# Kernel tuning notes

Measured on AMD Instinct MI355X. Metric: run time of the kernel, lower is better.

## Reference

```python
import jax, jax.numpy as jnp
import numpy as np

B, N, C, K, RPE = 8, 4096, 256, 16, 64
LN_EPS = 1e-5


def _layernorm(x, g, b):
    m = jnp.mean(x, axis=-1, keepdims=True)
    v = jnp.mean((x - m) ** 2, axis=-1, keepdims=True)
    return (x - m) * jax.lax.rsqrt(v + LN_EPS) * g + b


def setup_inputs() -> dict:
    key = jax.random.key(0)
    ks = jax.random.split(key, 10)
    def w(k, shape, s=0.02):
        return jax.random.normal(k, shape, jnp.float32) * s
    return {
        "x": jax.random.normal(ks[0], (B, N, C), jnp.float32),
        "pos": jax.random.normal(ks[1], (B, N, 3), jnp.float32),
        "Wq": w(ks[2], (C, C)),
        "Wk": w(ks[3], (C, C)),
        "Wv": w(ks[4], (C, C)),
        "W1": w(ks[5], (3, RPE)), "b1": jnp.zeros((RPE,), jnp.float32),
        "W2": w(ks[6], (RPE, C)), "b2": jnp.zeros((C,), jnp.float32),
        "Wp": w(ks[7], (C, C)), "bp": jnp.zeros((C,), jnp.float32),
        "gq": jnp.ones((C,), jnp.float32), "betaq": jnp.zeros((C,), jnp.float32),
        "gkv": jnp.ones((C,), jnp.float32), "betakv": jnp.zeros((C,), jnp.float32),
    }


def reference(x, pos, Wq, Wk, Wv, W1, b1, W2, b2, Wp, bp, gq, betaq, gkv, betakv):
    scale = C ** (-0.5)
    x_q = _layernorm(x, gq, betaq)
    x_kv = _layernorm(x, gkv, betakv)
    q = x_q @ Wq                      # (B,N,C)
    k = x_kv @ Wk                     # (B,N,C)
    v = x_kv @ Wv                     # (B,N,C)

    # kNN over squared pairwise distances (self has distance 0 on the diagonal)
    a2 = jnp.sum(pos * pos, axis=-1)                       # (B,N)
    dist2 = a2[:, :, None] + a2[:, None, :] - 2.0 * jnp.einsum(
        "bnc,bmc->bnm", pos, pos)                          # (B,N,N)
    dist2 = jnp.maximum(dist2, 0.0)
    eye = jnp.eye(N, dtype=bool)
    dist2 = jnp.where(eye[None], 0.0, dist2)
    _, idx = jax.lax.top_k(-dist2, K)                      # (B,N,K) smallest-k

    gather = jax.vmap(lambda f, i: f[i])                   # (N,C),(N,K)->(N,K,C)
    k_nb = gather(k, idx)                                  # (B,N,K,C)
    v_nb = gather(v, idx)                                  # (B,N,K,C)
    pos_nb = gather(pos, idx)                              # (B,N,K,3)

    rel = pos[:, :, None, :] - pos_nb                      # (B,N,K,3)
    rel_enc = jax.nn.relu(rel @ W1 + b1) @ W2 + b2         # (B,N,K,C)

    attn_logits = jnp.einsum("bnc,bnkc->bnk", q, k_nb) * scale
    attn_logits = attn_logits + jnp.sum(rel_enc, axis=-1) * scale
    attn = jax.nn.softmax(attn_logits, axis=-1)            # (B,N,K)

    out = jnp.einsum("bnk,bnkc->bnc", attn, v_nb)
    out = out @ Wp + bp
    return out
```

## Files before the change

### kernel.cpp

```cpp
#include <hip/hip_runtime.h>
#include <hip/hip_bf16.h>
#include <stdint.h>

#define Bv 8
#define Nv 4096
#define Cv 256
#define Kv 16
#define RPEv 64
#define CAPv 160

typedef short bf16x8 __attribute__((ext_vector_type(8)));
typedef float f32x4 __attribute__((ext_vector_type(4)));
typedef _Float16 half2v __attribute__((ext_vector_type(2)));
typedef unsigned short u16x2 __attribute__((ext_vector_type(2)));

static __device__ __forceinline__ float bf2f(unsigned int u16) {
    union { unsigned int i; float f; } v; v.i = u16 << 16; return v.f;
}
static __device__ __forceinline__ unsigned short f2bf(float f) {
    union { float f; unsigned int i; } v; v.f = f;
    unsigned int x = v.i;
    return (unsigned short)((x + 0x7fffu + ((x >> 16) & 1u)) >> 16);
}
static __device__ __forceinline__ unsigned int umin32(unsigned int a, unsigned int b) { return a < b ? a : b; }
static __device__ __forceinline__ unsigned int umax32(unsigned int a, unsigned int b) { return a > b ? a : b; }
static __device__ __forceinline__ unsigned short f2h(float f) {
    _Float16 h = (_Float16)f; return __builtin_bit_cast(unsigned short, h);
}
static __device__ __forceinline__ float h2f(unsigned int u) {
    _Float16 h = __builtin_bit_cast(_Float16, (unsigned short)(u & 0xffffu)); return (float)h;
}
static __device__ __forceinline__ half2v bch2(unsigned int u) { return __builtin_bit_cast(half2v, u); }
static __device__ __forceinline__ unsigned int bcu32(u16x2 v) { return __builtin_bit_cast(unsigned int, v); }

__global__ __launch_bounds__(256) void pre_kernel(
    const float* __restrict__ x,
    const float* __restrict__ gq, const float* __restrict__ bq,
    const float* __restrict__ gkv, const float* __restrict__ bkv,
    unsigned short* __restrict__ Aq, unsigned short* __restrict__ Akv,
    const float* __restrict__ Wq, const float* __restrict__ Wk,
    const float* __restrict__ Wv, const float* __restrict__ Wp,
    unsigned short* __restrict__ Bt,
    const float* __restrict__ W2, const float* __restrict__ b2,
    float* __restrict__ w2sum, float* __restrict__ b2sum)
{
    const int bid = blockIdx.x;
    const int tid = threadIdx.x;
    if (bid < 4096) {
        const long r0 = (long)bid * 8;
        const int row = tid >> 5;
        const int c0 = (tid & 31) * 8;
        const float* xr = x + (r0 + row) * Cv + c0;
        float xv[8];
        *(float4*)&xv[0] = *(const float4*)xr;
        *(float4*)&xv[4] = *(const float4*)(xr + 4);
        float s = 0.f, s2 = 0.f;
#pragma unroll
        for (int i = 0; i < 8; ++i) { s += xv[i]; s2 = fmaf(xv[i], xv[i], s2); }
#pragma unroll
        for (int m = 16; m >= 1; m >>= 1) { s += __shfl_xor(s, m); s2 += __shfl_xor(s2, m); }
        const float mean = s * (1.f / Cv);
        const float var = fmaf(-mean, mean, s2 * (1.f / Cv));
        const float rs = rsqrtf(fmaxf(var, 0.f) + 1e-5f);
        unsigned int pq[4], pk[4];
#pragma unroll
        for (int i = 0; i < 4; ++i) {
            const int c = c0 + 2 * i;
            const float h0 = (xv[2 * i] - mean) * rs;
            const float h1 = (xv[2 * i + 1] - mean) * rs;
            const unsigned int q0 = f2bf(fmaf(h0, gq[c], bq[c]));
            const unsigned int q1 = f2bf(fmaf(h1, gq[c + 1], bq[c + 1]));
            const unsigned int k0 = f2bf(fmaf(h0, gkv[c], bkv[c]));
            const unsigned int k1 = f2bf(fmaf(h1, gkv[c + 1], bkv[c + 1]));
            pq[i] = q0 | (q1 << 16);
            pk[i] = k0 | (k1 << 16);
        }
        const long off = (r0 + row) * Cv + c0;
        *(uint4*)&Aq[off]  = make_uint4(pq[0], pq[1], pq[2], pq[3]);
        *(uint4*)&Akv[off] = make_uint4(pk[0], pk[1], pk[2], pk[3]);
    } else if (bid < 5120) {
        const int r = bid - 4096;
        const float* W = (r < 256) ? Wq : (r < 512) ? Wk : (r < 768) ? Wv : Wp;
        const int n = r & 255;
        Bt[r * 256 + tid] = f2bf(W[tid * 256 + n]);
    } else {
        if (tid < RPEv) {
            float s = 0.f;
            for (int c = 0; c < Cv; ++c) s += W2[tid * Cv + c];
            w2sum[tid] = s;
        }
        if (tid == 0) {
            float s = 0.f;
            for (int c = 0; c < Cv; ++c) s += b2[c];
            *b2sum = s;
        }
    }
}

__global__ __launch_bounds__(256) void gemmknn_kernel(
    const float* __restrict__ pos, int* __restrict__ idx_out,
    const unsigned short* __restrict__ Aq, const unsigned short* __restrict__ Akv,
    const unsigned short* __restrict__ Bt,
    unsigned short* __restrict__ qo, unsigned short* __restrict__ ko,
    unsigned short* __restrict__ vo)
{
    __shared__ char smem[65536] __attribute__((aligned(16)));
    const int tid = threadIdx.x;
    const int bid = blockIdx.x;

    if (bid < 1024) {
        uint2* pxy2 = (uint2*)smem;
        unsigned int* pz2 = (unsigned int*)(smem + 16384);
        uint4* qu = (uint4*)(smem + 24576);
        unsigned int* akeys = (unsigned int*)(smem + 25088);
        unsigned int* cnt = (unsigned int*)(smem + 28160);
        unsigned short* bufs = (unsigned short*)(smem + 28288);

        const int ql = tid >> 3;
        const int s  = tid & 7;
        const int q  = bid * 32 + ql;
        const int b  = q >> 12;
        const int n  = q & (Nv - 1);
        const float* pb = pos + (size_t)b * Nv * 3;

        for (int i = tid; i < Nv / 2; i += 256) {
            const float* pp = pb + 6 * i;
            const float2 u0 = *(const float2*)pp;
            const float2 u1 = *(const float2*)(pp + 2);
            const float2 u2 = *(const float2*)(pp + 4);
            const unsigned int x0 = f2h(u0.x), y0 = f2h(u0.y), z0 = f2h(u1.x);
            const unsigned int x1 = f2h(u1.y), y1 = f2h(u2.x), z1 = f2h(u2.y);
            pxy2[i] = make_uint2(x0 | (x1 << 16), y0 | (y1 << 16));
            pz2[i] = z0 | (z1 << 16);
        }
        __syncthreads();

        const int pq = n >> 1;
        const int hq = (n & 1) * 16;
        const uint2 qxy = pxy2[pq];
        const unsigned int qzz = pz2[pq];
        const unsigned int hx = (qxy.x >> hq) & 0xffffu;
        const unsigned int hy = (qxy.y >> hq) & 0xffffu;
        const unsigned int hz = (qzz   >> hq) & 0xffffu;
        const half2v qxp = bch2(hx | (hx << 16));
        const half2v qyp = bch2(hy | (hy << 16));
        const half2v qzp = bch2(hz | (hz << 16));

        u16x2 ch0 = {0x7c00, 0x7c00}, ch1 = ch0, ch2 = ch0;
        for (int t = 0; t < 256; ++t) {
            const int p = 8 * t + s;
            const uint2 xy = pxy2[p];
            const unsigned int zz = pz2[p];
            const half2v dx = bch2(xy.x) - qxp;
            const half2v dy = bch2(xy.y) - qyp;
            const half2v dz = bch2(zz) - qzp;
            const half2v d2 = dx * dx + dy * dy + dz * dz;
            const u16x2 k = __builtin_bit_cast(u16x2, d2);
            const u16x2 mn0 = __builtin_elementwise_min(ch0, k);
            const u16x2 mx0 = __builtin_elementwise_max(ch0, k);
            ch0 = mn0;
            const u16x2 mn1 = __builtin_elementwise_min(ch1, mx0);
            const u16x2 mx1 = __builtin_elementwise_max(ch1, mx0);
            ch1 = mn1;
            ch2 = __builtin_elementwise_min(ch2, mx1);
        }
        akeys[tid * 3 + 0] = bcu32(ch0);
        akeys[tid * 3 + 1] = bcu32(ch1);
        akeys[tid * 3 + 2] = bcu32(ch2);
        __syncthreads();

        if (tid < 32) {
            unsigned int sel16[16];
#pragma unroll
            for (int i = 0; i < 16; ++i) sel16[i] = 0xFFFFFFFFu;
            for (int s8 = 0; s8 < 8; ++s8) {
#pragma unroll
                for (int i3 = 0; i3 < 3; ++i3) {
                    const unsigned int v = akeys[(8 * tid + s8) * 3 + i3];
#pragma unroll
                    for (int h = 0; h < 2; ++h) {
                        unsigned int cand = (h == 0) ? (v & 0xffffu) : (v >> 16);
                        if (cand < sel16[15]) {
#pragma unroll
                            for (int i = 0; i < 16; ++i) {
                                const unsigned int lo = umin32(sel16[i], cand);
                                cand = umax32(sel16[i], cand);
                                sel16[i] = lo;
                            }
                        }
                    }
                }
            }
            const float tauf = h2f(sel16[15]) * 1.12f + 1e-9f;
            const unsigned int taub = f2h(tauf);
            const int n2 = (bid * 32 + tid) & (Nv - 1);
            const int pq2 = n2 >> 1;
            const int hq2 = (n2 & 1) * 16;
            const uint2 qxy2 = pxy2[pq2];
            const unsigned int qzz2 = pz2[pq2];
            const unsigned int hx2 = (qxy2.x >> hq2) & 0xffffu;
            const unsigned int hy2 = (qxy2.y >> hq2) & 0xffffu;
            const unsigned int hz2 = (qzz2   >> hq2) & 0xffffu;
            qu[tid] = make_uint4(hx2 | (hx2 << 16), hy2 | (hy2 << 16),
                                 hz2 | (hz2 << 16), taub);
            cnt[tid] = 0;
        }
        __syncthreads();

        uint2 cxy[8]; unsigned int czp[8];
#pragma unroll
        for (int k = 0; k < 8; ++k) {
            cxy[k] = pxy2[tid + (k << 8)];
            czp[k] = pz2[tid + (k << 8)];
        }
        for (int q2 = 0; q2 < 32; ++q2) {
            const uint4 Q = qu[q2];
            const half2v Qx = bch2(Q.x), Qy = bch2(Q.y), Qz = bch2(Q.z);
            const unsigned int taub = Q.w;
#pragma unroll
            for (int k = 0; k < 8; ++k) {
                const half2v dx = bch2(cxy[k].x) - Qx;
                const half2v dy = bch2(cxy[k].y) - Qy;
                const half2v dz = bch2(czp[k]) - Qz;
                const half2v d2 = dx * dx + dy * dy + dz * dz;
                const unsigned int bits = __builtin_bit_cast(unsigned int, d2);
                const unsigned int lo = bits & 0xffffu;
                const unsigned int hi = bits >> 16;
                const int p = tid + (k << 8);
                if (lo < taub) {
                    const unsigned int slot = atomicAdd(&cnt[q2], 1u);
                    if (slot < CAPv) bufs[q2 * CAPv + slot] = (unsigned short)(2 * p);
                }
                if (hi < taub) {
                    const unsigned int slot = atomicAdd(&cnt[q2], 1u);
                    if (slot < CAPv) bufs[q2 * CAPv + slot] = (unsigned short)(2 * p + 1);
                }
            }
        }
        __syncthreads();

        if (tid < 32) {
            const int q2 = bid * 32 + tid;
            const int n2 = q2 & (Nv - 1);
            const int b2 = q2 >> 12;
            const float* pb2 = pos + (size_t)b2 * Nv * 3;
            const double qxd = (double)pb2[3 * n2];
            const double qyd = (double)pb2[3 * n2 + 1];
            const double qzd = (double)pb2[3 * n2 + 2];
            const double a2qd = qxd * qxd + qyd * qyd + qzd * qzd;
            int c = (int)cnt[tid]; if (c > CAPv) c = CAPv;
            unsigned long long sel[Kv];
#pragma unroll
            for (int i = 0; i < Kv; ++i) sel[i] = ~0ull;
            for (int t = 0; t < c; ++t) {
                const int j = bufs[tid * CAPv + t];
                const double cxd = (double)pb2[3 * j];
                const double cyd = (double)pb2[3 * j + 1];
                const double czd = (double)pb2[3 * j + 2];
                const double a2cd = cxd * cxd + cyd * cyd + czd * czd;
                const double ddot = qxd * cxd + qyd * cyd + qzd * czd;
                double dv = (a2qd + a2cd) - 2.0 * ddot;
                dv = (dv < 0.0) ? 0.0 : dv;
                if (j == n2) dv = 0.0;
                union { double d; unsigned long long u; } cv; cv.d = dv;
                const unsigned long long key = (cv.u & ~0xFFFULL) | (unsigned long long)j;
                if (key < sel[Kv - 1]) {
                    unsigned long long cc = key;
#pragma unroll
                    for (int i = 0; i < Kv; ++i) {
                        const unsigned long long lo = (sel[i] < cc) ? sel[i] : cc;
                        const unsigned long long hi = (sel[i] < cc) ? cc : sel[i];
                        sel[i] = lo; cc = hi;
                    }
                }
            }
#pragma unroll
            for (int i = 0; i < Kv; ++i)
                idx_out[(long)q2 * Kv + i] = (int)(sel[i] & 0xFFFull);
        }
        return;
    }

    {
        unsigned short (*Albs)[128 * 64] = (unsigned short (*)[128 * 64])smem;
        unsigned short (*Blbs)[128 * 64] = (unsigned short (*)[128 * 64])(smem + 32768);

        const int gb = bid - 1024;
        const int rt = gb & 255;
        const int ct = gb >> 8;
        const unsigned short* A = (ct < 2) ? Aq : Akv;
        const int mat = ct >> 1;
        unsigned short* outp = (mat == 0) ? qo : (mat == 1) ? ko : vo;
        const int colInMat = (ct & 1) * 128;

        const int wid = tid >> 6, l = tid & 63;
        const int wr = wid >> 1, wc = wid & 1;

        int srow[4], scol8[4];
#pragma unroll
        for (int it = 0; it < 4; ++it) {
            const int chunk = it * 256 + tid;
            srow[it] = chunk >> 3;
            scol8[it] = ((chunk & 7) ^ (srow[it] & 7)) * 8;
        }

#define STAGE(buf, ks)                                                                  \
    {                                                                                   \
        _Pragma("unroll")                                                               \
        for (int it = 0; it < 4; ++it) {                                                \
            const unsigned short* ga = A + ((size_t)(rt * 128 + srow[it])) * 256        \
                                         + (ks) * 64 + scol8[it];                       \
            const unsigned short* gb_ = Bt + ((size_t)(ct * 128 + srow[it])) * 256      \
                                           + (ks) * 64 + scol8[it];                     \
            __builtin_amdgcn_global_load_lds(                                           \
                (const __attribute__((address_space(1))) unsigned int*)(const void*)ga, \
                (__attribute__((address_space(3))) unsigned int*)(void*)                \
                    ((char*)&Albs[buf][0] + (it * 256 + tid) * 16), 16, 0, 0);          \
            __builtin_amdgcn_global_load_lds(                                           \
                (const __attribute__((address_space(1))) unsigned int*)(const void*)gb_,\
                (__attribute__((address_space(3))) unsigned int*)(void*)                \
                    ((char*)&Blbs[buf][0] + (it * 256 + tid) * 16), 16, 0, 0);          \
        }                                                                               \
    }

        f32x4 acc[4][4];
#pragma unroll
        for (int m = 0; m < 4; ++m)
#pragma unroll
            for (int n = 0; n < 4; ++n) acc[m][n] = (f32x4){0.f, 0.f, 0.f, 0.f};

        STAGE(0, 0);
        __syncthreads();

        for (int ks = 0; ks < 4; ++ks) {
            const int cur = ks & 1;
            if (ks < 3) STAGE(cur ^ 1, ks + 1);
#pragma unroll
            for (int kk = 0; kk < 2; ++kk) {
                bf16x8 a[4], b[4];
#pragma unroll
                for (int m = 0; m < 4; ++m) {
                    const int row = wr * 64 + m * 16 + (l & 15);
                    const int byte = row * 128 + ((((kk * 4 + (l >> 4)) * 16)) ^ ((row & 7) << 4));
                    a[m] = *(const bf16x8*)((const char*)&Albs[cur][0] + byte);
                }
#pragma unroll
                for (int n = 0; n < 4; ++n) {
                    const int row = wc * 64 + n * 16 + (l & 15);
                    const int byte = row * 128 + ((((kk * 4 + (l >> 4)) * 16)) ^ ((row & 7) << 4));
                    b[n] = *(const bf16x8*)((const char*)&Blbs[cur][0] + byte);
                }
#pragma unroll
                for (int m = 0; m < 4; ++m)
#pragma unroll
                    for (int n = 0; n < 4; ++n)
                        acc[m][n] = __builtin_amdgcn_mfma_f32_16x16x32_bf16(a[m], b[n], acc[m][n], 0, 0, 0);
            }
            __syncthreads();
        }

#pragma unroll
        for (int m = 0; m < 4; ++m) {
#pragma unroll
            for (int n = 0; n < 4; ++n) {
#pragma unroll
                for (int j = 0; j < 4; ++j) {
                    const int row = rt * 128 + wr * 64 + m * 16 + (l >> 4) * 4 + j;
                    const int col = colInMat + wc * 64 + n * 16 + (l & 15);
                    outp[(size_t)row * 256 + col] = f2bf(acc[m][n][j]);
                }
            }
        }
#undef STAGE
    }
}

__global__ __launch_bounds__(256) void gemm_proj_kernel(
    const unsigned short* __restrict__ Ab, const unsigned short* __restrict__ Btp,
    const float* __restrict__ bp, float* __restrict__ out)
{
    __shared__ unsigned short Albs[2][128 * 64];
    __shared__ unsigned short Blbs[2][128 * 64];

    const int tid = threadIdx.x;
    const int rt = blockIdx.x;
    const int ct = blockIdx.y;

    const int wid = tid >> 6, l = tid & 63;
    const int wr = wid >> 1, wc = wid & 1;

    int srow[4], scol8[4];
#pragma unroll
    for (int it = 0; it < 4; ++it) {
        const int chunk = it * 256 + tid;
        srow[it] = chunk >> 3;
        scol8[it] = ((chunk & 7) ^ (srow[it] & 7)) * 8;
    }

#define STAGE(buf, ks)                                                                  \
    {                                                                                   \
        _Pragma("unroll")                                                               \
        for (int it = 0; it < 4; ++it) {                                                \
            const unsigned short* ga = Ab + ((size_t)(rt * 128 + srow[it])) * 256       \
                                          + (ks) * 64 + scol8[it];                      \
            const unsigned short* gb = Btp + ((size_t)(ct * 128 + srow[it])) * 256      \
                                           + (ks) * 64 + scol8[it];                     \
            __builtin_amdgcn_global_load_lds(                                           \
                (const __attribute__((address_space(1))) unsigned int*)(const void*)ga, \
                (__attribute__((address_space(3))) unsigned int*)(void*)                \
                    ((char*)&Albs[buf][0] + (it * 256 + tid) * 16), 16, 0, 0);          \
            __builtin_amdgcn_global_load_lds(                                           \
                (const __attribute__((address_space(1))) unsigned int*)(const void*)gb, \
                (__attribute__((address_space(3))) unsigned int*)(void*)                \
                    ((char*)&Blbs[buf][0] + (it * 256 + tid) * 16), 16, 0, 0);          \
        }                                                                               \
    }

    f32x4 acc[4][4];
#pragma unroll
    for (int m = 0; m < 4; ++m)
#pragma unroll
        for (int n = 0; n < 4; ++n) acc[m][n] = (f32x4){0.f, 0.f, 0.f, 0.f};

    STAGE(0, 0);
    __syncthreads();

    for (int ks = 0; ks < 4; ++ks) {
        const int cur = ks & 1;
        if (ks < 3) STAGE(cur ^ 1, ks + 1);
#pragma unroll
        for (int kk = 0; kk < 2; ++kk) {
            bf16x8 a[4], b[4];
#pragma unroll
            for (int m = 0; m < 4; ++m) {
                const int row = wr * 64 + m * 16 + (l & 15);
                const int byte = row * 128 + ((((kk * 4 + (l >> 4)) * 16)) ^ ((row & 7) << 4));
                a[m] = *(const bf16x8*)((const char*)&Albs[cur][0] + byte);
            }
#pragma unroll
            for (int n = 0; n < 4; ++n) {
                const int row = wc * 64 + n * 16 + (l & 15);
                const int byte = row * 128 + ((((kk * 4 + (l >> 4)) * 16)) ^ ((row & 7) << 4));
                b[n] = *(const bf16x8*)((const char*)&Blbs[cur][0] + byte);
            }
#pragma unroll
            for (int m = 0; m < 4; ++m)
#pragma unroll
                for (int n = 0; n < 4; ++n)
                    acc[m][n] = __builtin_amdgcn_mfma_f32_16x16x32_bf16(a[m], b[n], acc[m][n], 0, 0, 0);
        }
        __syncthreads();
    }

#pragma unroll
    for (int n = 0; n < 4; ++n) {
        const int col = ct * 128 + wc * 64 + n * 16 + (l & 15);
        const float bpv = bp[col];
#pragma unroll
        for (int m = 0; m < 4; ++m) {
#pragma unroll
            for (int j = 0; j < 4; ++j) {
                const int row = rt * 128 + wr * 64 + m * 16 + (l >> 4) * 4 + j;
                out[(size_t)row * 256 + col] = acc[m][n][j] + bpv;
            }
        }
    }
#undef STAGE
}

__global__ __launch_bounds__(256) void attn_core_kernel(
    unsigned short* __restrict__ qb, const unsigned short* __restrict__ kb,
    const unsigned short* __restrict__ vb, const int* __restrict__ idx,
    const float* __restrict__ pos, const float* __restrict__ W1,
    const float* __restrict__ b1, const float* __restrict__ w2sum,
    const float* __restrict__ b2sum)
{
    __shared__ float q_lds[8][Cv];
    __shared__ float lg[8][Kv];
    __shared__ float wgt[8][Kv];
    __shared__ int idx_l[8][Kv];
    __shared__ float W1l[3 * RPEv];
    __shared__ float b1l[RPEv], w2s[RPEv];
    __shared__ float posq[24];
    __shared__ float b2s_l;

    const int tid = threadIdx.x;
    const long r0 = (long)blockIdx.x * 8;
    const int bq = (int)(r0 >> 12);

    {
        float* ql = &q_lds[0][0];
        for (int i = tid; i < 8 * Cv; i += 256) ql[i] = bf2f(qb[r0 * Cv + i]);
    }
    if (tid < 128) ((int*)idx_l)[tid] = idx[r0 * Kv + tid];
    if (tid < 3 * RPEv) W1l[tid] = W1[tid];
    if (tid < RPEv) { b1l[tid] = b1[tid]; w2s[tid] = w2sum[tid]; }
    if (tid < 24) posq[tid] = pos[r0 * 3 + tid];
    if (tid == 0) b2s_l = *b2sum;
    __syncthreads();

    const int g = tid >> 4, l = tid & 15;
    for (int r = 0; r < 8; ++r) {
        const int nb = idx_l[r][g];
        const long gi = (long)bq * Nv + nb;
        const unsigned short* kr = kb + gi * Cv + l * 16;
        const float* qq = &q_lds[r][l * 16];
        const uint4 kA = *(const uint4*)kr;
        const uint4 kB = *(const uint4*)(kr + 8);
        float part = 0.f;
        part = fmaf(qq[0],  bf2f(kA.x & 0xffffu), part);
        part = fmaf(qq[1],  bf2f(kA.x >> 16),     part);
        part = fmaf(qq[2],  bf2f(kA.y & 0xffffu), part);
        part = fmaf(qq[3],  bf2f(kA.y >> 16),     part);
        part = fmaf(qq[4],  bf2f(kA.z & 0xffffu), part);
        part = fmaf(qq[5],  bf2f(kA.z >> 16),     part);
        part = fmaf(qq[6],  bf2f(kA.w & 0xffffu), part);
        part = fmaf(qq[7],  bf2f(kA.w >> 16),     part);
        part = fmaf(qq[8],  bf2f(kB.x & 0xffffu), part);
        part = fmaf(qq[9],  bf2f(kB.x >> 16),     part);
        part = fmaf(qq[10], bf2f(kB.y & 0xffffu), part);
        part = fmaf(qq[11], bf2f(kB.y >> 16),     part);
        part = fmaf(qq[12], bf2f(kB.z & 0xffffu), part);
        part = fmaf(qq[13], bf2f(kB.z >> 16),     part);
        part = fmaf(qq[14], bf2f(kB.w & 0xffffu), part);
        part = fmaf(qq[15], bf2f(kB.w >> 16),     part);
        const float rx = posq[r * 3 + 0] - pos[gi * 3 + 0];
        const float ry = posq[r * 3 + 1] - pos[gi * 3 + 1];
        const float rz = posq[r * 3 + 2] - pos[gi * 3 + 2];
#pragma unroll
        for (int u4 = 0; u4 < 4; ++u4) {
            const int u = l * 4 + u4;
            float h = fmaf(rx, W1l[u], fmaf(ry, W1l[RPEv + u], fmaf(rz, W1l[2 * RPEv + u], b1l[u])));
            h = fmaxf(h, 0.f);
            part = fmaf(h, w2s[u], part);
        }
        part += __shfl_xor(part, 8);
        part += __shfl_xor(part, 4);
        part += __shfl_xor(part, 2);
        part += __shfl_xor(part, 1);
        if (l == 0) lg[r][g] = (part + b2s_l) * 0.0625f;
    }
    __syncthreads();
    if (tid < 128) {
        const int rr = tid >> 4, gg = tid & 15;
        const float v = lg[rr][gg];
        float m = v;
        m = fmaxf(m, __shfl_xor(m, 8)); m = fmaxf(m, __shfl_xor(m, 4));
        m = fmaxf(m, __shfl_xor(m, 2)); m = fmaxf(m, __shfl_xor(m, 1));
        const float e = __expf(v - m);
        float ssum = e;
        ssum += __shfl_xor(ssum, 8); ssum += __shfl_xor(ssum, 4);
        ssum += __shfl_xor(ssum, 2); ssum += __shfl_xor(ssum, 1);
        wgt[rr][gg] = e / ssum;
    }
    __syncthreads();
    {
        const int c = tid;
        for (int r = 0; r < 8; ++r) {
            float acc = 0.f;
#pragma unroll
            for (int t = 0; t < Kv; ++t) {
                const long gi = (long)bq * Nv + idx_l[r][t];
                acc = fmaf(wgt[r][t], bf2f((unsigned)vb[gi * Cv + c]), acc);
            }
            qb[(r0 + r) * Cv + c] = f2bf(acc);
        }
    }
}

extern "C" void kernel_launch(void* const* d_in, const int* in_sizes, int n_in,
                              void* d_out, int out_size, void* d_ws, size_t ws_size,
                              hipStream_t stream) {
    (void)in_sizes; (void)n_in; (void)out_size; (void)ws_size;
    const float* x      = (const float*)d_in[0];
    const float* pos    = (const float*)d_in[1];
    const float* Wq     = (const float*)d_in[2];
    const float* Wk     = (const float*)d_in[3];
    const float* Wv     = (const float*)d_in[4];
    const float* W1     = (const float*)d_in[5];
    const float* b1     = (const float*)d_in[6];
    const float* W2     = (const float*)d_in[7];
    const float* b2     = (const float*)d_in[8];
    const float* Wp     = (const float*)d_in[9];
    const float* bp     = (const float*)d_in[10];
    const float* gq     = (const float*)d_in[11];
    const float* betaq  = (const float*)d_in[12];
    const float* gkv    = (const float*)d_in[13];
    const float* betakv = (const float*)d_in[14];
    float* out = (float*)d_out;

    char* ws = (char*)d_ws;
    unsigned short* qb = (unsigned short*)(ws);
    unsigned short* kb = (unsigned short*)(ws + 16777216);
    unsigned short* vb = (unsigned short*)(ws + 33554432);
    int*   idx   = (int*)  (ws + 50331648);
    unsigned short* Bt = (unsigned short*)(ws + 52428800);
    float* w2sum = (float*)(ws + 52953088);
    float* b2sum = (float*)(ws + 52953344);

    unsigned short* Aq  = (unsigned short*)d_out;
    unsigned short* Akv = (unsigned short*)d_out + 8388608;

    hipLaunchKernelGGL(pre_kernel, dim3(5121), dim3(256), 0, stream,
                       x, gq, betaq, gkv, betakv, Aq, Akv,
                       Wq, Wk, Wv, Wp, Bt, W2, b2, w2sum, b2sum);
    hipLaunchKernelGGL(gemmknn_kernel, dim3(2560), dim3(256), 0, stream,
                       pos, idx, Aq, Akv, Bt, qb, kb, vb);
    hipLaunchKernelGGL(attn_core_kernel, dim3(4096), dim3(256), 0, stream,
                       qb, kb, vb, idx, pos, W1, b1, w2sum, b2sum);
    hipLaunchKernelGGL(gemm_proj_kernel, dim3(256, 2), dim3(256), 0, stream,
                       qb, Bt + 768 * 256, bp, out);
}
```

Baseline: 230.5 us.

## Move kNN candidate filtering into preprocessing kernel and split exact selection out

```diff
diff --git a/kernel.cpp b/kernel.cpp
--- a/kernel.cpp
+++ b/kernel.cpp
@@ -33,7 +33,7 @@
 static __device__ __forceinline__ half2v bch2(unsigned int u) { return __builtin_bit_cast(half2v, u); }
 static __device__ __forceinline__ unsigned int bcu32(u16x2 v) { return __builtin_bit_cast(unsigned int, v); }
 
-__global__ __launch_bounds__(256) void pre_kernel(
+__global__ __launch_bounds__(256) void preknn_kernel(
     const float* __restrict__ x,
     const float* __restrict__ gq, const float* __restrict__ bq,
     const float* __restrict__ gkv, const float* __restrict__ bkv,
@@ -42,73 +42,17 @@
     const float* __restrict__ Wv, const float* __restrict__ Wp,
     unsigned short* __restrict__ Bt,
     const float* __restrict__ W2, const float* __restrict__ b2,
-    float* __restrict__ w2sum, float* __restrict__ b2sum)
+    float* __restrict__ w2sum, float* __restrict__ b2sum,
+    const float* __restrict__ pos,
+    unsigned int* __restrict__ gcnt, unsigned short* __restrict__ gbufs)
 {
-    const int bid = blockIdx.x;
-    const int tid = threadIdx.x;
-    if (bid < 4096) {
-        const long r0 = (long)bid * 8;
-        const int row = tid >> 5;
-        const int c0 = (tid & 31) * 8;
-        const float* xr = x + (r0 + row) * Cv + c0;
-        float xv[8];
-        *(float4*)&xv[0] = *(const float4*)xr;
-        *(float4*)&xv[4] = *(const float4*)(xr + 4);
-        float s = 0.f, s2 = 0.f;
-#pragma unroll
-        for (int i = 0; i < 8; ++i) { s += xv[i]; s2 = fmaf(xv[i], xv[i], s2); }
-#pragma unroll
-        for (int m = 16; m >= 1; m >>= 1) { s += __shfl_xor(s, m); s2 += __shfl_xor(s2, m); }
-        const float mean = s * (1.f / Cv);
-        const float var = fmaf(-mean, mean, s2 * (1.f / Cv));
-        const float rs = rsqrtf(fmaxf(var, 0.f) + 1e-5f);
-        unsigned int pq[4], pk[4];
-#pragma unroll
-        for (int i = 0; i < 4; ++i) {
-            const int c = c0 + 2 * i;
-            const float h0 = (xv[2 * i] - mean) * rs;
-            const float h1 = (xv[2 * i + 1] - mean) * rs;
-            const unsigned int q0 = f2bf(fmaf(h0, gq[c], bq[c]));
-            const unsigned int q1 = f2bf(fmaf(h1, gq[c + 1], bq[c + 1]));
-            const unsigned int k0 = f2bf(fmaf(h0, gkv[c], bkv[c]));
-            const unsigned int k1 = f2bf(fmaf(h1, gkv[c + 1], bkv[c + 1]));
-            pq[i] = q0 | (q1 << 16);
-            pk[i] = k0 | (k1 << 16);
-        }
-        const long off = (r0 + row) * Cv + c0;
-        *(uint4*)&Aq[off]  = make_uint4(pq[0], pq[1], pq[2], pq[3]);
-        *(uint4*)&Akv[off] = make_uint4(pk[0], pk[1], pk[2], pk[3]);
-    } else if (bid < 5120) {
-        const int r = bid - 4096;
-        const float* W = (r < 256) ? Wq : (r < 512) ? Wk : (r < 768) ? Wv : Wp;
-        const int n = r & 255;
-        Bt[r * 256 + tid] = f2bf(W[tid * 256 + n]);
-    } else {
-        if (tid < RPEv) {
-            float s = 0.f;
-            for (int c = 0; c < Cv; ++c) s += W2[tid * Cv + c];
-            w2sum[tid] = s;
-        }
-        if (tid == 0) {
-            float s = 0.f;
-            for (int c = 0; c < Cv; ++c) s += b2[c];
-            *b2sum = s;
-        }
-    }
-}
-
-__global__ __launch_bounds__(256) void gemmknn_kernel(
-    const float* __restrict__ pos, int* __restrict__ idx_out,
-    const unsigned short* __restrict__ Aq, const unsigned short* __restrict__ Akv,
-    const unsigned short* __restrict__ Bt,
-    unsigned short* __restrict__ qo, unsigned short* __restrict__ ko,
-    unsigned short* __restrict__ vo)
-{
-    __shared__ char smem[65536] __attribute__((aligned(16)));
+    __shared__ char smem[38912] __attribute__((aligned(16)));
     const int tid = threadIdx.x;
     const int bid = blockIdx.x;
-
-    if (bid < 1024) {
+    const bool isKnn = ((bid % 6) == 0) && (bid < 6144);
+
+    if (isKnn) {
+        const int knn_id = bid / 6;
         uint2* pxy2 = (uint2*)smem;
         unsigned int* pz2 = (unsigned int*)(smem + 16384);
         uint4* qu = (uint4*)(smem + 24576);
@@ -118,7 +62,7 @@
 
         const int ql = tid >> 3;
         const int s  = tid & 7;
-        const int q  = bid * 32 + ql;
+        const int q  = knn_id * 32 + ql;
         const int b  = q >> 12;
         const int n  = q & (Nv - 1);
         const float* pb = pos + (size_t)b * Nv * 3;
@@ -193,7 +137,7 @@
             }
             const float tauf = h2f(sel16[15]) * 1.12f + 1e-9f;
             const unsigned int taub = f2h(tauf);
-            const int n2 = (bid * 32 + tid) & (Nv - 1);
+            const int n2 = (knn_id * 32 + tid) & (Nv - 1);
             const int pq2 = n2 >> 1;
             const int hq2 = (n2 & 1) * 16;
             const uint2 qxy2 = pxy2[pq2];
@@ -239,70 +183,136 @@
         }
         __syncthreads();
 
-        if (tid < 32) {
-            const int q2 = bid * 32 + tid;
-            const int n2 = q2 & (Nv - 1);
-            const int b2 = q2 >> 12;
-            const float* pb2 = pos + (size_t)b2 * Nv * 3;
-            const double qxd = (double)pb2[3 * n2];
-            const double qyd = (double)pb2[3 * n2 + 1];
-            const double qzd = (double)pb2[3 * n2 + 2];
-            const double a2qd = qxd * qxd + qyd * qyd + qzd * qzd;
-            int c = (int)cnt[tid]; if (c > CAPv) c = CAPv;
-            unsigned long long sel[Kv];
-#pragma unroll
-            for (int i = 0; i < Kv; ++i) sel[i] = ~0ull;
-            for (int t = 0; t < c; ++t) {
-                const int j = bufs[tid * CAPv + t];
-                const double cxd = (double)pb2[3 * j];
-                const double cyd = (double)pb2[3 * j + 1];
-                const double czd = (double)pb2[3 * j + 2];
-                const double a2cd = cxd * cxd + cyd * cyd + czd * czd;
-                const double ddot = qxd * cxd + qyd * cyd + qzd * czd;
-                double dv = (a2qd + a2cd) - 2.0 * ddot;
-                dv = (dv < 0.0) ? 0.0 : dv;
-                if (j == n2) dv = 0.0;
-                union { double d; unsigned long long u; } cv; cv.d = dv;
-                const unsigned long long key = (cv.u & ~0xFFFULL) | (unsigned long long)j;
-                if (key < sel[Kv - 1]) {
-                    unsigned long long cc = key;
-#pragma unroll
-                    for (int i = 0; i < Kv; ++i) {
-                        const unsigned long long lo = (sel[i] < cc) ? sel[i] : cc;
-                        const unsigned long long hi = (sel[i] < cc) ? cc : sel[i];
-                        sel[i] = lo; cc = hi;
-                    }
-                }
-            }
-#pragma unroll
-            for (int i = 0; i < Kv; ++i)
-                idx_out[(long)q2 * Kv + i] = (int)(sel[i] & 0xFFFull);
-        }
+        const int qb0 = knn_id * 32;
+        if (tid < 32) gcnt[qb0 + tid] = umin32(cnt[tid], CAPv);
+        for (int i = tid; i < 32 * CAPv; i += 256)
+            gbufs[(size_t)qb0 * CAPv + i] = bufs[i];
         return;
     }
 
-    {
-        unsigned short (*Albs)[128 * 64] = (unsigned short (*)[128 * 64])smem;
-        unsigned short (*Blbs)[128 * 64] = (unsigned short (*)[128 * 64])(smem + 32768);
-
-        const int gb = bid - 1024;
-        const int rt = gb & 255;
-        const int ct = gb >> 8;
-        const unsigned short* A = (ct < 2) ? Aq : Akv;
-        const int mat = ct >> 1;
-        unsigned short* outp = (mat == 0) ? qo : (mat == 1) ? ko : vo;
-        const int colInMat = (ct & 1) * 128;
-
-        const int wid = tid >> 6, l = tid & 63;
-        const int wr = wid >> 1, wc = wid & 1;
-
-        int srow[4], scol8[4];
-#pragma unroll
-        for (int it = 0; it < 4; ++it) {
-            const int chunk = it * 256 + tid;
-            srow[it] = chunk >> 3;
-            scol8[it] = ((chunk & 7) ^ (srow[it] & 7)) * 8;
-        }
+    const int pid = bid - 1 - (bid - 1) / 6;
+    if (pid < 4096) {
+        const long r0 = (long)pid * 8;
+        const int row = tid >> 5;
+        const int c0 = (tid & 31) * 8;
+        const float* xr = x + (r0 + row) * Cv + c0;
+        float xv[8];
+        *(float4*)&xv[0] = *(const float4*)xr;
+        *(float4*)&xv[4] = *(const float4*)(xr + 4);
+        float s = 0.f, s2 = 0.f;
+#pragma unroll
+        for (int i = 0; i < 8; ++i) { s += xv[i]; s2 = fmaf(xv[i], xv[i], s2); }
+#pragma unroll
+        for (int m = 16; m >= 1; m >>= 1) { s += __shfl_xor(s, m); s2 += __shfl_xor(s2, m); }
+        const float mean = s * (1.f / Cv);
+        const float var = fmaf(-mean, mean, s2 * (1.f / Cv));
+        const float rs = rsqrtf(fmaxf(var, 0.f) + 1e-5f);
+        unsigned int pq[4], pk[4];
+#pragma unroll
+        for (int i = 0; i < 4; ++i) {
+            const int c = c0 + 2 * i;
+            const float h0 = (xv[2 * i] - mean) * rs;
+            const float h1 = (xv[2 * i + 1] - mean) * rs;
+            const unsigned int q0 = f2bf(fmaf(h0, gq[c], bq[c]));
+            const unsigned int q1 = f2bf(fmaf(h1, gq[c + 1], bq[c + 1]));
+            const unsigned int k0 = f2bf(fmaf(h0, gkv[c], bkv[c]));
+            const unsigned int k1 = f2bf(fmaf(h1, gkv[c + 1], bkv[c + 1]));
+            pq[i] = q0 | (q1 << 16);
+            pk[i] = k0 | (k1 << 16);
+        }
+        const long off = (r0 + row) * Cv + c0;
+        *(uint4*)&Aq[off]  = make_uint4(pq[0], pq[1], pq[2], pq[3]);
+        *(uint4*)&Akv[off] = make_uint4(pk[0], pk[1], pk[2], pk[3]);
+    } else if (pid < 5120) {
+        const int r = pid - 4096;
+        const float* W = (r < 256) ? Wq : (r < 512) ? Wk : (r < 768) ? Wv : Wp;
+        const int n = r & 255;
+        Bt[r * 256 + tid] = f2bf(W[tid * 256 + n]);
+    } else {
+        if (tid < RPEv) {
+            float s = 0.f;
+            for (int c = 0; c < Cv; ++c) s += W2[tid * Cv + c];
+            w2sum[tid] = s;
+        }
+        if (tid == 0) {
+            float s = 0.f;
+            for (int c = 0; c < Cv; ++c) s += b2[c];
+            *b2sum = s;
+        }
+    }
+}
+
+__global__ __launch_bounds__(256) void kselect_kernel(
+    const float* __restrict__ pos, const unsigned int* __restrict__ gcnt,
+    const unsigned short* __restrict__ gbufs, int* __restrict__ idx_out)
+{
+    const int t = blockIdx.x * 256 + threadIdx.x;
+    const int n2 = t & (Nv - 1);
+    const int b2 = t >> 12;
+    const float* pb2 = pos + (size_t)b2 * Nv * 3;
+    const double qxd = (double)pb2[3 * n2];
+    const double qyd = (double)pb2[3 * n2 + 1];
+    const double qzd = (double)pb2[3 * n2 + 2];
+    const double a2qd = qxd * qxd + qyd * qyd + qzd * qzd;
+    int c = (int)gcnt[t]; if (c > CAPv) c = CAPv;
+    const unsigned short* myb = gbufs + (size_t)t * CAPv;
+    unsigned long long sel[Kv];
+#pragma unroll
+    for (int i = 0; i < Kv; ++i) sel[i] = ~0ull;
+    for (int s = 0; s < c; ++s) {
+        const int j = myb[s];
+        const double cxd = (double)pb2[3 * j];
+        const double cyd = (double)pb2[3 * j + 1];
+        const double czd = (double)pb2[3 * j + 2];
+        const double a2cd = cxd * cxd + cyd * cyd + czd * czd;
+        const double ddot = qxd * cxd + qyd * cyd + qzd * czd;
+        double dv = (a2qd + a2cd) - 2.0 * ddot;
+        dv = (dv < 0.0) ? 0.0 : dv;
+        if (j == n2) dv = 0.0;
+        union { double d; unsigned long long u; } cv; cv.d = dv;
+        const unsigned long long key = (cv.u & ~0xFFFULL) | (unsigned long long)j;
+        if (key < sel[Kv - 1]) {
+            unsigned long long cc = key;
+#pragma unroll
+            for (int i = 0; i < Kv; ++i) {
+                const unsigned long long lo = (sel[i] < cc) ? sel[i] : cc;
+                const unsigned long long hi = (sel[i] < cc) ? cc : sel[i];
+                sel[i] = lo; cc = hi;
+            }
+        }
+    }
+#pragma unroll
+    for (int i = 0; i < Kv; ++i)
+        idx_out[(long)t * Kv + i] = (int)(sel[i] & 0xFFFull);
+}
+
+__global__ __launch_bounds__(256) void gemm_qkv_kernel(
+    const unsigned short* __restrict__ Aq, const unsigned short* __restrict__ Akv,
+    const unsigned short* __restrict__ Bt,
+    unsigned short* __restrict__ qo, unsigned short* __restrict__ ko,
+    unsigned short* __restrict__ vo)
+{
+    __shared__ unsigned short Albs[2][128 * 64];
+    __shared__ unsigned short Blbs[2][128 * 64];
+
+    const int tid = threadIdx.x;
+    const int rt = blockIdx.x;
+    const int ct = blockIdx.y;
+    const unsigned short* A = (ct < 2) ? Aq : Akv;
+    const int mat = ct >> 1;
+    unsigned short* outp = (mat == 0) ? qo : (mat == 1) ? ko : vo;
+    const int colInMat = (ct & 1) * 128;
+
+    const int wid = tid >> 6, l = tid & 63;
+    const int wr = wid >> 1, wc = wid & 1;
+
+    int srow[4], scol8[4];
+#pragma unroll
+    for (int it = 0; it < 4; ++it) {
+        const int chunk = it * 256 + tid;
+        srow[it] = chunk >> 3;
+        scol8[it] = ((chunk & 7) ^ (srow[it] & 7)) * 8;
+    }
 
 #define STAGE(buf, ks)                                                                  \
     {                                                                                   \
@@ -310,69 +320,68 @@
         for (int it = 0; it < 4; ++it) {                                                \
             const unsigned short* ga = A + ((size_t)(rt * 128 + srow[it])) * 256        \
                                          + (ks) * 64 + scol8[it];                       \
-            const unsigned short* gb_ = Bt + ((size_t)(ct * 128 + srow[it])) * 256      \
-                                           + (ks) * 64 + scol8[it];                     \
+            const unsigned short* gb = Bt + ((size_t)(ct * 128 + srow[it])) * 256       \
+                                          + (ks) * 64 + scol8[it];                      \
             __builtin_amdgcn_global_load_lds(                                           \
                 (const __attribute__((address_space(1))) unsigned int*)(const void*)ga, \
                 (__attribute__((address_space(3))) unsigned int*)(void*)                \
                     ((char*)&Albs[buf][0] + (it * 256 + tid) * 16), 16, 0, 0);          \
             __builtin_amdgcn_global_load_lds(                                           \
-                (const __attribute__((address_space(1))) unsigned int*)(const void*)gb_,\
+                (const __attribute__((address_space(1))) unsigned int*)(const void*)gb, \
                 (__attribute__((address_space(3))) unsigned int*)(void*)                \
                     ((char*)&Blbs[buf][0] + (it * 256 + tid) * 16), 16, 0, 0);          \
         }                                                                               \
     }
 
-        f32x4 acc[4][4];
-#pragma unroll
-        for (int m = 0; m < 4; ++m)
-#pragma unroll
-            for (int n = 0; n < 4; ++n) acc[m][n] = (f32x4){0.f, 0.f, 0.f, 0.f};
-
-        STAGE(0, 0);
+    f32x4 acc[4][4];
+#pragma unroll
+    for (int m = 0; m < 4; ++m)
+#pragma unroll
+        for (int n = 0; n < 4; ++n) acc[m][n] = (f32x4){0.f, 0.f, 0.f, 0.f};
+
+    STAGE(0, 0);
+    __syncthreads();
+
+    for (int ks = 0; ks < 4; ++ks) {
+        const int cur = ks & 1;
+        if (ks < 3) STAGE(cur ^ 1, ks + 1);
+#pragma unroll
+        for (int kk = 0; kk < 2; ++kk) {
+            bf16x8 a[4], b[4];
+#pragma unroll
+            for (int m = 0; m < 4; ++m) {
+                const int row = wr * 64 + m * 16 + (l & 15);
+                const int byte = row * 128 + ((((kk * 4 + (l >> 4)) * 16)) ^ ((row & 7) << 4));
+                a[m] = *(const bf16x8*)((const char*)&Albs[cur][0] + byte);
+            }
+#pragma unroll
+            for (int n = 0; n < 4; ++n) {
+                const int row = wc * 64 + n * 16 + (l & 15);
+                const int byte = row * 128 + ((((kk * 4 + (l >> 4)) * 16)) ^ ((row & 7) << 4));
+                b[n] = *(const bf16x8*)((const char*)&Blbs[cur][0] + byte);
+            }
+#pragma unroll
+            for (int m = 0; m < 4; ++m)
+#pragma unroll
+                for (int n = 0; n < 4; ++n)
+                    acc[m][n] = __builtin_amdgcn_mfma_f32_16x16x32_bf16(a[m], b[n], acc[m][n], 0, 0, 0);
+        }
         __syncthreads();
-
-        for (int ks = 0; ks < 4; ++ks) {
-            const int cur = ks & 1;
-            if (ks < 3) STAGE(cur ^ 1, ks + 1);
-#pragma unroll
-            for (int kk = 0; kk < 2; ++kk) {
-                bf16x8 a[4], b[4];
-#pragma unroll
-                for (int m = 0; m < 4; ++m) {
-                    const int row = wr * 64 + m * 16 + (l & 15);
-                    const int byte = row * 128 + ((((kk * 4 + (l >> 4)) * 16)) ^ ((row & 7) << 4));
-                    a[m] = *(const bf16x8*)((const char*)&Albs[cur][0] + byte);
-                }
-#pragma unroll
-                for (int n = 0; n < 4; ++n) {
-                    const int row = wc * 64 + n * 16 + (l & 15);
-                    const int byte = row * 128 + ((((kk * 4 + (l >> 4)) * 16)) ^ ((row & 7) << 4));
-                    b[n] = *(const bf16x8*)((const char*)&Blbs[cur][0] + byte);
-                }
-#pragma unroll
-                for (int m = 0; m < 4; ++m)
-#pragma unroll
-                    for (int n = 0; n < 4; ++n)
-                        acc[m][n] = __builtin_amdgcn_mfma_f32_16x16x32_bf16(a[m], b[n], acc[m][n], 0, 0, 0);
-            }
-            __syncthreads();
-        }
-
-#pragma unroll
-        for (int m = 0; m < 4; ++m) {
-#pragma unroll
-            for (int n = 0; n < 4; ++n) {
-#pragma unroll
-                for (int j = 0; j < 4; ++j) {
-                    const int row = rt * 128 + wr * 64 + m * 16 + (l >> 4) * 4 + j;
-                    const int col = colInMat + wc * 64 + n * 16 + (l & 15);
-                    outp[(size_t)row * 256 + col] = f2bf(acc[m][n][j]);
-                }
-            }
-        }
+    }
+
+#pragma unroll
+    for (int m = 0; m < 4; ++m) {
+#pragma unroll
+        for (int n = 0; n < 4; ++n) {
+#pragma unroll
+            for (int j = 0; j < 4; ++j) {
+                const int row = rt * 128 + wr * 64 + m * 16 + (l >> 4) * 4 + j;
+                const int col = colInMat + wc * 64 + n * 16 + (l & 15);
+                outp[(size_t)row * 256 + col] = f2bf(acc[m][n][j]);
+            }
+        }
+    }
 #undef STAGE
-    }
 }
 
 __global__ __launch_bounds__(256) void gemm_proj_kernel(
@@ -598,14 +607,20 @@
     float* w2sum = (float*)(ws + 52953088);
     float* b2sum = (float*)(ws + 52953344);
 
+    unsigned short* gbufs = qb;
+    unsigned int*   gcnt  = (unsigned int*)kb;
+
     unsigned short* Aq  = (unsigned short*)d_out;
     unsigned short* Akv = (unsigned short*)d_out + 8388608;
 
-    hipLaunchKernelGGL(pre_kernel, dim3(5121), dim3(256), 0, stream,
+    hipLaunchKernelGGL(preknn_kernel, dim3(6145), dim3(256), 0, stream,
                        x, gq, betaq, gkv, betakv, Aq, Akv,
-                       Wq, Wk, Wv, Wp, Bt, W2, b2, w2sum, b2sum);
-    hipLaunchKernelGGL(gemmknn_kernel, dim3(2560), dim3(256), 0, stream,
-                       pos, idx, Aq, Akv, Bt, qb, kb, vb);
+                       Wq, Wk, Wv, Wp, Bt, W2, b2, w2sum, b2sum,
+                       pos, gcnt, gbufs);
+    hipLaunchKernelGGL(kselect_kernel, dim3(128), dim3(256), 0, stream,
+                       pos, gcnt, gbufs, idx);
+    hipLaunchKernelGGL(gemm_qkv_kernel, dim3(256, 6), dim3(256), 0, stream,
+                       Aq, Akv, Bt, qb, kb, vb);
     hipLaunchKernelGGL(attn_core_kernel, dim3(4096), dim3(256), 0, stream,
                        qb, kb, vb, idx, pos, W1, b1, w2sum, b2sum);
     hipLaunchKernelGGL(gemm_proj_kernel, dim3(256, 2), dim3(256), 0, stream,
```

New measurement: 266.3 us. +15.5%, slower.
